# Optimization experiments

Hardware: AMD Instinct MI355X
Metric: run time of the kernel (lower is better)

Reference implementation:

```python
import jax, jax.numpy as jnp
import numpy as np

B, S, D_MODEL, D_K, D_V = 8, 2048, 1024, 512, 512


def setup_inputs() -> dict:
    key = jax.random.key(0)
    ks = jax.random.split(key, 7)
    sq = jax.random.normal(ks[0], (B, S, D_MODEL), dtype=jnp.float32)
    skv = jax.random.normal(ks[1], (B, S, D_MODEL), dtype=jnp.float32)
    q_pad = jax.random.uniform(ks[2], (B, S)) < 0.1
    kv_pad = jax.random.uniform(ks[3], (B, S)) < 0.1
    Wq = jax.random.normal(ks[4], (D_MODEL, D_K), dtype=jnp.float32) * (D_MODEL ** -0.5)
    Wk = jax.random.normal(ks[5], (D_MODEL, D_K), dtype=jnp.float32) * (D_MODEL ** -0.5)
    Wv = jax.random.normal(ks[6], (D_MODEL, D_V), dtype=jnp.float32) * (D_MODEL ** -0.5)
    return {
        "source_query": sq,
        "source_key_value": skv,
        "source_query_padding_mask": q_pad,
        "source_key_value_padding_mask": kv_pad,
        "Wq": Wq,
        "Wk": Wk,
        "Wv": Wv,
    }


def reference(source_query, source_key_value, source_query_padding_mask,
              source_key_value_padding_mask, Wq, Wk, Wv):
    neg_inf = jnp.float32(-jnp.inf)
    q = source_query @ Wq          # [B,Sq,d_k]
    k = source_key_value @ Wk      # [B,Sk,d_k]
    v = source_key_value @ Wv      # [B,Sk,d_v]
    scale = jnp.float32(D_K) ** -0.5
    scores = jnp.einsum("bqd,bkd->bqk", q, k) * scale  # [B,Sq,Sk]
    # query padding mask broadcast along key dim, kv padding mask along query dim
    pad = source_query_padding_mask[:, :, None] | source_key_value_padding_mask[:, None, :]
    scores = jnp.where(pad, neg_inf, scores)
    # causal mask (masked=True): positions above diagonal blocked
    Sq = scores.shape[1]
    causal = jnp.tril(jnp.ones((Sq, Sq), dtype=bool))
    scores = jnp.where(causal[None, :, :], scores, neg_inf)
    attn = jax.nn.softmax(scores, axis=-1)
    # fully-masked rows produce NaN -> zero (matches torch nan masked_fill)
    attn = jnp.where(jnp.isnan(attn), jnp.float32(0.0), attn)
    # dropout p=0.0 (eval): identity
    out = jnp.einsum("bqk,bkv->bqv", attn, v)  # [B,Sq,d_v]
    return out
```

## Files before the change

kernel.cpp:

```cpp
#include <hip/hip_runtime.h>

typedef unsigned short u16;
typedef unsigned int   u32;
typedef __attribute__((ext_vector_type(4))) float  f32x4;
typedef __attribute__((ext_vector_type(8))) __bf16 bf16x8;

#define BATCH 8
#define SEQ   2048
#define DMODEL 1024
#define DK    512
#define DV    512
#define SCALE 0.044194173824159216f

__device__ __forceinline__ u16 f2bf(float f) {
  u32 u = __float_as_uint(f);
  return (u16)((u + 0x7fffu + ((u >> 16) & 1u)) >> 16);
}

__device__ __forceinline__ bool read_mask(const void* p, int idx, int mode) {
  if (mode == 1) return ((const unsigned char*)p)[idx] != 0;
  if (mode == 2) return ((const float*)p)[idx] != 0.0f;
  return ((const int*)p)[idx] != 0;
}

__device__ __forceinline__ void gl_lds16(const u16* g, u16* l) {
  __builtin_amdgcn_global_load_lds(
      (const __attribute__((address_space(1))) u32*)g,
      (__attribute__((address_space(3))) u32*)l, 16, 0, 0);
}

__global__ void detect_mode(const int* __restrict__ qp, int* __restrict__ flag) {
  __shared__ int f;
  if (threadIdx.x == 0) f = 0;
  __syncthreads();
  int local = 0;
  for (int i = threadIdx.x; i < 4096; i += 256) {
    int v = qp[i];
    if (v == 0x3F800000) local |= 2;
    else if (v != 0 && v != 1 && v != -1) local |= 1;
  }
  if (local) atomicOr(&f, local);
  __syncthreads();
  if (threadIdx.x == 0) {
    int m = 0;
    if (f & 2) m = 2; else if (f & 1) m = 1;
    *flag = m;
  }
}

__global__ __launch_bounds__(256) void wt_transpose(const float* __restrict__ W0,
                                                    const float* __restrict__ W1,
                                                    const float* __restrict__ W2,
                                                    u16* __restrict__ dst) {
  const float* W = (blockIdx.z == 0) ? W0 : (blockIdx.z == 1) ? W1 : W2;
  u16* out = dst + (size_t)blockIdx.z * (DK * DMODEL);
  __shared__ float T[32][33];
  int k0 = blockIdx.x * 32, n0 = blockIdx.y * 32;
  int tx = threadIdx.x, ty = threadIdx.y;
#pragma unroll
  for (int i = 0; i < 4; ++i) {
    int r = ty + i * 8;
    T[r][tx] = W[(size_t)(k0 + r) * DK + n0 + tx];
  }
  __syncthreads();
#pragma unroll
  for (int i = 0; i < 4; ++i) {
    int r = ty + i * 8;
    out[(size_t)(n0 + r) * DMODEL + k0 + tx] = f2bf(T[tx][r]);
  }
}

__global__ __launch_bounds__(256) void convert_bf16(const float* __restrict__ src,
                                                    u16* __restrict__ dst) {
  int i = (blockIdx.x * 256 + threadIdx.x) * 8;
  f32x4 a = *(const f32x4*)(src + i);
  f32x4 b = *(const f32x4*)(src + i + 4);
  uint4 o;
  o.x = (u32)f2bf(a[0]) | ((u32)f2bf(a[1]) << 16);
  o.y = (u32)f2bf(a[2]) | ((u32)f2bf(a[3]) << 16);
  o.z = (u32)f2bf(b[0]) | ((u32)f2bf(b[1]) << 16);
  o.w = (u32)f2bf(b[2]) | ((u32)f2bf(b[3]) << 16);
  *(uint4*)(dst + i) = o;
}

__global__ __launch_bounds__(256, 3) void proj_gemm(const u16* __restrict__ A,
                                                    const u16* __restrict__ Wt_base,
                                                    int z0, u16* __restrict__ dst0,
                                                    u16* __restrict__ dst1) {
  int z = z0 + blockIdx.z;
  const u16* Wt = Wt_base + (size_t)z * (DK * DMODEL);
  u16* dst = (z == 2) ? dst1 : dst0;
  int n0 = blockIdx.x * 128, m0 = blockIdx.y * 128;

  __shared__ __align__(16) u16 As[128 * 64];
  __shared__ __align__(16) u16 Bs[128 * 64];

  int tid = threadIdx.x, lane = tid & 63, w = tid >> 6;
  int wm = w & 1, wn = w >> 1;
  int l15 = lane & 15, lg = lane >> 4;
  int r3 = lane >> 3, c7 = lane & 7;
  int csw = c7 ^ r3;

  f32x4 acc[4][4];
#pragma unroll
  for (int m = 0; m < 4; ++m)
#pragma unroll
    for (int n = 0; n < 4; ++n) acc[m][n] = (f32x4)0.0f;

  for (int k0 = 0; k0 < DMODEL; k0 += 64) {
    __syncthreads();
#pragma unroll
    for (int u = 0; u < 4; ++u) {
      int t = w * 4 + u;
      gl_lds16(A  + (size_t)(m0 + t * 8 + r3) * DMODEL + k0 + csw * 8, &As[t * 512]);
      gl_lds16(Wt + (size_t)(n0 + t * 8 + r3) * DMODEL + k0 + csw * 8, &Bs[t * 512]);
    }
    __syncthreads();
#pragma unroll
    for (int ks = 0; ks < 2; ++ks) {
      bf16x8 af[4], bfv[4];
#pragma unroll
      for (int m = 0; m < 4; ++m) {
        int row = wm * 64 + m * 16 + l15;
        af[m] = *(const bf16x8*)&As[row * 64 + (((ks * 4 + lg) ^ (l15 & 7)) * 8)];
      }
#pragma unroll
      for (int n = 0; n < 4; ++n) {
        int row = wn * 64 + n * 16 + l15;
        bfv[n] = *(const bf16x8*)&Bs[row * 64 + (((ks * 4 + lg) ^ (l15 & 7)) * 8)];
      }
#pragma unroll
      for (int m = 0; m < 4; ++m)
#pragma unroll
        for (int n = 0; n < 4; ++n)
          acc[m][n] = __builtin_amdgcn_mfma_f32_16x16x32_bf16(af[m], bfv[n], acc[m][n], 0, 0, 0);
    }
  }

  if (z != 2) {
#pragma unroll
    for (int m = 0; m < 4; ++m) {
      int rowb = m0 + wm * 64 + m * 16;
#pragma unroll
      for (int n = 0; n < 4; ++n) {
        int col = n0 + wn * 64 + n * 16 + l15;
        size_t base = (size_t)(rowb >> 4) * 8192 + (size_t)(col >> 5) * 512 + (col & 31);
#pragma unroll
        for (int r = 0; r < 4; ++r)
          dst[base + (lg * 4 + r) * 32] = f2bf(acc[m][n][r]);
      }
    }
  } else {
#pragma unroll
    for (int m = 0; m < 4; ++m) {
      int row0 = m0 + wm * 64 + m * 16 + lg * 4;
      int b = row0 >> 11, s0 = row0 & 2047;
#pragma unroll
      for (int n = 0; n < 4; ++n) {
        int dv = n0 + wn * 64 + n * 16 + l15;
        size_t off = (size_t)b * (SEQ * DV) + (size_t)(dv >> 4) * 32768 +
                     (size_t)(s0 >> 5) * 512 + (dv & 15) * 32 + (s0 & 31);
        u16 tmp[4] __attribute__((aligned(8)));
#pragma unroll
        for (int r = 0; r < 4; ++r) tmp[r] = f2bf(acc[m][n][r]);
        *(uint2*)&dst[off] = *(const uint2*)tmp;
      }
    }
  }
}

__global__ __launch_bounds__(256, 2) void attn_kernel(
    const u16* __restrict__ Qf, const u16* __restrict__ Kf,
    const u16* __restrict__ Vf, const void* __restrict__ qpad,
    const void* __restrict__ kvpad, const int* __restrict__ flag,
    float* __restrict__ out) {
  __shared__ __align__(16) u16 Pbuf[32 * 72];
  __shared__ float partm[32 * 2];
  __shared__ float ald[32];
  __shared__ float partl[32 * 2];

  int tid = threadIdx.x;
  int lane = tid & 63, w = tid >> 6;
  int l15 = lane & 15, lg = lane >> 4;
  int wk = w & 1;
  int m  = w >> 1;
  int bi = blockIdx.x;
  int j = bi & 63, b = bi >> 6;
  int qt = (j & 1) ? (63 - (j >> 1)) : (j >> 1);
  int q0 = qt * 32;
  int mode = *flag;
  int lanoff = l15 * 32 + lg * 8;

  const u16* Qb = Qf + (size_t)b * (SEQ * DK);
  const u16* Kb = Kf + (size_t)b * (SEQ * DK);
  const u16* Vb = Vf + (size_t)b * (SEQ * DV);

  bf16x8 qf[16];
  {
    const u16* qp = Qb + (size_t)(qt * 2 + m) * 8192 + lanoff;
#pragma unroll
    for (int ks = 0; ks < 16; ++ks) qf[ks] = *(const bf16x8*)(qp + ks * 512);
  }

  f32x4 o[2][8];
#pragma unroll
  for (int m2 = 0; m2 < 2; ++m2)
#pragma unroll
    for (int n = 0; n < 8; ++n) o[m2][n] = (f32x4)0.0f;

  float mo[4], lsum[4];
#pragma unroll
  for (int r = 0; r < 4; ++r) { mo[r] = -1e38f; lsum[r] = 0.0f; }

  int nkt = (q0 + 95) >> 6;

  for (int kt = 0; kt < nkt; ++kt) {
    int k0 = kt * 64;

    f32x4 s0 = (f32x4)0.0f, s1 = (f32x4)0.0f;
    {
      const u16* kp0 = Kb + (size_t)((k0 >> 4) + wk * 2) * 8192 + lanoff;
      const u16* kp1 = kp0 + 8192;
#pragma unroll
      for (int ks = 0; ks < 16; ++ks) {
        bf16x8 b0 = *(const bf16x8*)(kp0 + ks * 512);
        bf16x8 b1 = *(const bf16x8*)(kp1 + ks * 512);
        s0 = __builtin_amdgcn_mfma_f32_16x16x32_bf16(qf[ks], b0, s0, 0, 0, 0);
        s1 = __builtin_amdgcn_mfma_f32_16x16x32_bf16(qf[ks], b1, s1, 0, 0, 0);
      }
    }

    float sv[2][4];
#pragma unroll
    for (int kg = 0; kg < 2; ++kg) {
      int key = k0 + wk * 32 + kg * 16 + l15;
      bool kvm = read_mask(kvpad, b * SEQ + key, mode);
#pragma unroll
      for (int r = 0; r < 4; ++r) {
        int qrow = q0 + m * 16 + lg * 4 + r;
        float x = (kg == 0 ? s0[r] : s1[r]) * SCALE;
        sv[kg][r] = (kvm || key > qrow) ? -__builtin_inff() : x;
      }
    }

    float wmax[4];
#pragma unroll
    for (int r = 0; r < 4; ++r) wmax[r] = fmaxf(sv[0][r], sv[1][r]);
#pragma unroll
    for (int d = 1; d < 16; d <<= 1)
#pragma unroll
      for (int r = 0; r < 4; ++r) wmax[r] = fmaxf(wmax[r], __shfl_xor(wmax[r], d));
    if (l15 == 0) {
#pragma unroll
      for (int r = 0; r < 4; ++r) partm[(m * 16 + lg * 4 + r) * 2 + wk] = wmax[r];
    }
    __syncthreads();

    float al[4], ws[4];
#pragma unroll
    for (int r = 0; r < 4; ++r) {
      int row = m * 16 + lg * 4 + r;
      float tm = fmaxf(partm[row * 2], partm[row * 2 + 1]);
      float mn = fmaxf(mo[r], fmaxf(tm, -1e38f));
      al[r] = __expf(mo[r] - mn);
      mo[r] = mn;
      float p0 = __expf(sv[0][r] - mn);
      float p1 = __expf(sv[1][r] - mn);
      Pbuf[row * 72 + wk * 32 + l15] = f2bf(p0);
      Pbuf[row * 72 + wk * 32 + 16 + l15] = f2bf(p1);
      ws[r] = p0 + p1;
    }
#pragma unroll
    for (int d = 1; d < 16; d <<= 1)
#pragma unroll
      for (int r = 0; r < 4; ++r) ws[r] += __shfl_xor(ws[r], d);
#pragma unroll
    for (int r = 0; r < 4; ++r) lsum[r] = lsum[r] * al[r] + ws[r];
    if (wk == 0 && l15 == 0) {
#pragma unroll
      for (int r = 0; r < 4; ++r) ald[m * 16 + lg * 4 + r] = al[r];
    }
    __syncthreads();

    float ar[2][4];
#pragma unroll
    for (int m2 = 0; m2 < 2; ++m2)
#pragma unroll
      for (int r = 0; r < 4; ++r) ar[m2][r] = ald[m2 * 16 + lg * 4 + r];
#pragma unroll
    for (int m2 = 0; m2 < 2; ++m2)
#pragma unroll
      for (int n = 0; n < 8; ++n)
#pragma unroll
        for (int r = 0; r < 4; ++r) o[m2][n][r] *= ar[m2][r];

    {
      const u16* vpb = Vb + (size_t)(w * 8) * 32768 + (size_t)(k0 >> 5) * 512 + lanoff;
#pragma unroll
      for (int ks = 0; ks < 2; ++ks) {
        bf16x8 pa0 = *(const bf16x8*)&Pbuf[(l15) * 72 + ks * 32 + lg * 8];
        bf16x8 pa1 = *(const bf16x8*)&Pbuf[(16 + l15) * 72 + ks * 32 + lg * 8];
#pragma unroll
        for (int n = 0; n < 4; ++n) {
          bf16x8 bv0 = *(const bf16x8*)(vpb + (size_t)(n * 2) * 32768 + ks * 512);
          bf16x8 bv1 = *(const bf16x8*)(vpb + (size_t)(n * 2 + 1) * 32768 + ks * 512);
          o[0][n * 2]     = __builtin_amdgcn_mfma_f32_16x16x32_bf16(pa0, bv0, o[0][n * 2], 0, 0, 0);
          o[1][n * 2]     = __builtin_amdgcn_mfma_f32_16x16x32_bf16(pa1, bv0, o[1][n * 2], 0, 0, 0);
          o[0][n * 2 + 1] = __builtin_amdgcn_mfma_f32_16x16x32_bf16(pa0, bv1, o[0][n * 2 + 1], 0, 0, 0);
          o[1][n * 2 + 1] = __builtin_amdgcn_mfma_f32_16x16x32_bf16(pa1, bv1, o[1][n * 2 + 1], 0, 0, 0);
        }
      }
    }
  }

  if (l15 == 0) {
#pragma unroll
    for (int r = 0; r < 4; ++r) partl[(m * 16 + lg * 4 + r) * 2 + wk] = lsum[r];
  }
  __syncthreads();
  {
    float f[2][4];
#pragma unroll
    for (int m2 = 0; m2 < 2; ++m2)
#pragma unroll
      for (int r = 0; r < 4; ++r) {
        int row = m2 * 16 + lg * 4 + r;
        float l = partl[row * 2] + partl[row * 2 + 1];
        bool qp = read_mask(qpad, b * SEQ + q0 + row, mode);
        f[m2][r] = (l > 0.0f && !qp) ? 1.0f / l : 0.0f;
      }
#pragma unroll
    for (int m2 = 0; m2 < 2; ++m2)
#pragma unroll
      for (int n = 0; n < 8; ++n) {
        int dv = w * 128 + n * 16 + l15;
#pragma unroll
        for (int r = 0; r < 4; ++r) {
          int row = m2 * 16 + lg * 4 + r;
          out[(size_t)(b * SEQ + q0 + row) * DV + dv] = o[m2][n][r] * f[m2][r];
        }
      }
  }
}

extern "C" void kernel_launch(void* const* d_in, const int* in_sizes, int n_in,
                              void* d_out, int out_size, void* d_ws, size_t ws_size,
                              hipStream_t stream) {
  const float* sq  = (const float*)d_in[0];
  const float* skv = (const float*)d_in[1];
  const void* qp   = d_in[2];
  const void* kvp  = d_in[3];
  const float* Wq  = (const float*)d_in[4];
  const float* Wk  = (const float*)d_in[5];
  const float* Wv  = (const float*)d_in[6];
  char* ws = (char*)d_ws;

  u16* Abf = (u16*)ws;
  u16* Qf  = (u16*)(ws + 33554432);
  u16* Kf  = (u16*)(ws + 50331648);
  u16* Vf  = (u16*)(ws + 67108864);
  u16* Wt  = (u16*)(ws + 83886080);
  int* flag = (int*)(ws + 87031808);

  wt_transpose<<<dim3(32, 16, 3), dim3(32, 8, 1), 0, stream>>>(Wq, Wk, Wv, Wt);
  detect_mode<<<1, 256, 0, stream>>>((const int*)qp, flag);

  convert_bf16<<<8192, 256, 0, stream>>>(sq, Abf);
  proj_gemm<<<dim3(4, 128, 1), dim3(256), 0, stream>>>(Abf, Wt, 0, Qf, Qf);

  convert_bf16<<<8192, 256, 0, stream>>>(skv, Abf);
  proj_gemm<<<dim3(4, 128, 2), dim3(256), 0, stream>>>(Abf, Wt, 1, Kf, Vf);

  attn_kernel<<<dim3(512), dim3(256), 0, stream>>>(Qf, Kf, Vf, qp, kvp, flag,
                                                   (float*)d_out);
}
```

Baseline: 479.5 us.

## Split attention block across eight waves with Q staged in LDS

The attention kernel moves from 4 to 8 waves per block. Each wave now computes a 16-key slice of the score tile and a 64-column slice of the output, and the Q tile is staged once into shared memory via direct global-to-LDS loads instead of being held in registers per wave. Every wave recomputes the row rescale factors from the per-row partial maxima, which removes the separate alpha broadcast buffer. The batch-major block order is also replaced with an interleaved batch/tile mapping for load balance. This is meant to raise parallelism and lower register pressure, at the cost of more LDS traffic for Q and more block-wide barrier participants.

```diff
diff --git a/kernel.cpp b/kernel.cpp
--- a/kernel.cpp
+++ b/kernel.cpp
@@ -169,24 +169,25 @@
   }
 }
 
-__global__ __launch_bounds__(256, 2) void attn_kernel(
+__global__ __launch_bounds__(512, 4) void attn_kernel(
     const u16* __restrict__ Qf, const u16* __restrict__ Kf,
     const u16* __restrict__ Vf, const void* __restrict__ qpad,
     const void* __restrict__ kvpad, const int* __restrict__ flag,
     float* __restrict__ out) {
+  __shared__ __align__(16) u16 Qs[32 * 512];
   __shared__ __align__(16) u16 Pbuf[32 * 72];
-  __shared__ float partm[32 * 2];
-  __shared__ float ald[32];
-  __shared__ float partl[32 * 2];
+  __shared__ float partm[32 * 4];
+  __shared__ float partl[32 * 4];
 
   int tid = threadIdx.x;
   int lane = tid & 63, w = tid >> 6;
   int l15 = lane & 15, lg = lane >> 4;
-  int wk = w & 1;
-  int m  = w >> 1;
+  int wk = w & 3;
+  int m  = w >> 2;
   int bi = blockIdx.x;
-  int j = bi & 63, b = bi >> 6;
-  int qt = (j & 1) ? (63 - (j >> 1)) : (j >> 1);
+  int b = bi & 7, j = bi >> 3;
+  int c = j & 31, h = j >> 5;
+  int qt = ((c ^ h) & 1) ? (63 - c) : c;
   int q0 = qt * 32;
   int mode = *flag;
   int lanoff = l15 * 32 + lg * 8;
@@ -195,119 +196,123 @@
   const u16* Kb = Kf + (size_t)b * (SEQ * DK);
   const u16* Vb = Vf + (size_t)b * (SEQ * DV);
 
-  bf16x8 qf[16];
   {
-    const u16* qp = Qb + (size_t)(qt * 2 + m) * 8192 + lanoff;
-#pragma unroll
-    for (int ks = 0; ks < 16; ++ks) qf[ks] = *(const bf16x8*)(qp + ks * 512);
-  }
-
-  f32x4 o[2][8];
-#pragma unroll
-  for (int m2 = 0; m2 < 2; ++m2)
-#pragma unroll
-    for (int n = 0; n < 8; ++n) o[m2][n] = (f32x4)0.0f;
-
-  float mo[4], lsum[4];
-#pragma unroll
-  for (int r = 0; r < 4; ++r) { mo[r] = -1e38f; lsum[r] = 0.0f; }
+    const u16* qsrc = Qb + (size_t)qt * 16384 + lane * 8;
+#pragma unroll
+    for (int u = 0; u < 4; ++u) {
+      int i = w * 4 + u;
+      gl_lds16(qsrc + i * 512, &Qs[i * 512]);
+    }
+  }
+
+  f32x4 o[2][4];
+#pragma unroll
+  for (int mf = 0; mf < 2; ++mf)
+#pragma unroll
+    for (int n = 0; n < 4; ++n) o[mf][n] = (f32x4)0.0f;
+
+  float mo[2][4], lsum[4];
+#pragma unroll
+  for (int mf = 0; mf < 2; ++mf)
+#pragma unroll
+    for (int r = 0; r < 4; ++r) mo[mf][r] = -1e38f;
+#pragma unroll
+  for (int r = 0; r < 4; ++r) lsum[r] = 0.0f;
 
   int nkt = (q0 + 95) >> 6;
+  __syncthreads();
 
   for (int kt = 0; kt < nkt; ++kt) {
     int k0 = kt * 64;
-
-    f32x4 s0 = (f32x4)0.0f, s1 = (f32x4)0.0f;
+    int key = k0 + wk * 16 + l15;
+    bool kvm = read_mask(kvpad, b * SEQ + key, mode);
+
+    f32x4 sa = (f32x4)0.0f, sb = (f32x4)0.0f;
     {
-      const u16* kp0 = Kb + (size_t)((k0 >> 4) + wk * 2) * 8192 + lanoff;
-      const u16* kp1 = kp0 + 8192;
-#pragma unroll
-      for (int ks = 0; ks < 16; ++ks) {
-        bf16x8 b0 = *(const bf16x8*)(kp0 + ks * 512);
-        bf16x8 b1 = *(const bf16x8*)(kp1 + ks * 512);
-        s0 = __builtin_amdgcn_mfma_f32_16x16x32_bf16(qf[ks], b0, s0, 0, 0, 0);
-        s1 = __builtin_amdgcn_mfma_f32_16x16x32_bf16(qf[ks], b1, s1, 0, 0, 0);
-      }
-    }
-
-    float sv[2][4];
-#pragma unroll
-    for (int kg = 0; kg < 2; ++kg) {
-      int key = k0 + wk * 32 + kg * 16 + l15;
-      bool kvm = read_mask(kvpad, b * SEQ + key, mode);
-#pragma unroll
-      for (int r = 0; r < 4; ++r) {
-        int qrow = q0 + m * 16 + lg * 4 + r;
-        float x = (kg == 0 ? s0[r] : s1[r]) * SCALE;
-        sv[kg][r] = (kvm || key > qrow) ? -__builtin_inff() : x;
-      }
+      const u16* kp = Kb + (size_t)((k0 >> 4) + wk) * 8192 + lanoff;
+      const u16* qp = &Qs[m * 8192 + lanoff];
+#pragma unroll
+      for (int ks = 0; ks < 16; ks += 2) {
+        bf16x8 qv0 = *(const bf16x8*)(qp + ks * 512);
+        bf16x8 kv0 = *(const bf16x8*)(kp + ks * 512);
+        bf16x8 qv1 = *(const bf16x8*)(qp + (ks + 1) * 512);
+        bf16x8 kv1 = *(const bf16x8*)(kp + (ks + 1) * 512);
+        sa = __builtin_amdgcn_mfma_f32_16x16x32_bf16(qv0, kv0, sa, 0, 0, 0);
+        sb = __builtin_amdgcn_mfma_f32_16x16x32_bf16(qv1, kv1, sb, 0, 0, 0);
+      }
+    }
+
+    float sv[4];
+#pragma unroll
+    for (int r = 0; r < 4; ++r) {
+      int qrow = q0 + m * 16 + lg * 4 + r;
+      float x = (sa[r] + sb[r]) * SCALE;
+      sv[r] = (kvm || key > qrow) ? -__builtin_inff() : x;
     }
 
     float wmax[4];
 #pragma unroll
-    for (int r = 0; r < 4; ++r) wmax[r] = fmaxf(sv[0][r], sv[1][r]);
+    for (int r = 0; r < 4; ++r) wmax[r] = sv[r];
 #pragma unroll
     for (int d = 1; d < 16; d <<= 1)
 #pragma unroll
       for (int r = 0; r < 4; ++r) wmax[r] = fmaxf(wmax[r], __shfl_xor(wmax[r], d));
     if (l15 == 0) {
 #pragma unroll
-      for (int r = 0; r < 4; ++r) partm[(m * 16 + lg * 4 + r) * 2 + wk] = wmax[r];
+      for (int r = 0; r < 4; ++r) partm[(m * 16 + lg * 4 + r) * 4 + wk] = wmax[r];
     }
     __syncthreads();
 
-    float al[4], ws[4];
+    float al[2][4];
+#pragma unroll
+    for (int mf = 0; mf < 2; ++mf)
+#pragma unroll
+      for (int r = 0; r < 4; ++r) {
+        int row = mf * 16 + lg * 4 + r;
+        float tm = fmaxf(fmaxf(partm[row * 4 + 0], partm[row * 4 + 1]),
+                         fmaxf(partm[row * 4 + 2], partm[row * 4 + 3]));
+        float mn = fmaxf(mo[mf][r], fmaxf(tm, -1e38f));
+        al[mf][r] = __expf(mo[mf][r] - mn);
+        mo[mf][r] = mn;
+      }
+    float ws[4];
 #pragma unroll
     for (int r = 0; r < 4; ++r) {
       int row = m * 16 + lg * 4 + r;
-      float tm = fmaxf(partm[row * 2], partm[row * 2 + 1]);
-      float mn = fmaxf(mo[r], fmaxf(tm, -1e38f));
-      al[r] = __expf(mo[r] - mn);
-      mo[r] = mn;
-      float p0 = __expf(sv[0][r] - mn);
-      float p1 = __expf(sv[1][r] - mn);
-      Pbuf[row * 72 + wk * 32 + l15] = f2bf(p0);
-      Pbuf[row * 72 + wk * 32 + 16 + l15] = f2bf(p1);
-      ws[r] = p0 + p1;
+      float p = __expf(sv[r] - mo[m][r]);
+      Pbuf[row * 72 + wk * 16 + l15] = f2bf(p);
+      ws[r] = p;
     }
 #pragma unroll
     for (int d = 1; d < 16; d <<= 1)
 #pragma unroll
       for (int r = 0; r < 4; ++r) ws[r] += __shfl_xor(ws[r], d);
 #pragma unroll
-    for (int r = 0; r < 4; ++r) lsum[r] = lsum[r] * al[r] + ws[r];
-    if (wk == 0 && l15 == 0) {
-#pragma unroll
-      for (int r = 0; r < 4; ++r) ald[m * 16 + lg * 4 + r] = al[r];
-    }
+    for (int r = 0; r < 4; ++r) lsum[r] = lsum[r] * al[m][r] + ws[r];
     __syncthreads();
 
-    float ar[2][4];
-#pragma unroll
-    for (int m2 = 0; m2 < 2; ++m2)
-#pragma unroll
-      for (int r = 0; r < 4; ++r) ar[m2][r] = ald[m2 * 16 + lg * 4 + r];
-#pragma unroll
-    for (int m2 = 0; m2 < 2; ++m2)
-#pragma unroll
-      for (int n = 0; n < 8; ++n)
-#pragma unroll
-        for (int r = 0; r < 4; ++r) o[m2][n][r] *= ar[m2][r];
+#pragma unroll
+    for (int mf = 0; mf < 2; ++mf)
+#pragma unroll
+      for (int n = 0; n < 4; ++n)
+#pragma unroll
+        for (int r = 0; r < 4; ++r) o[mf][n][r] *= al[mf][r];
 
     {
-      const u16* vpb = Vb + (size_t)(w * 8) * 32768 + (size_t)(k0 >> 5) * 512 + lanoff;
+      bf16x8 pa0[2], pa1[2];
 #pragma unroll
       for (int ks = 0; ks < 2; ++ks) {
-        bf16x8 pa0 = *(const bf16x8*)&Pbuf[(l15) * 72 + ks * 32 + lg * 8];
-        bf16x8 pa1 = *(const bf16x8*)&Pbuf[(16 + l15) * 72 + ks * 32 + lg * 8];
-#pragma unroll
-        for (int n = 0; n < 4; ++n) {
-          bf16x8 bv0 = *(const bf16x8*)(vpb + (size_t)(n * 2) * 32768 + ks * 512);
-          bf16x8 bv1 = *(const bf16x8*)(vpb + (size_t)(n * 2 + 1) * 32768 + ks * 512);
-          o[0][n * 2]     = __builtin_amdgcn_mfma_f32_16x16x32_bf16(pa0, bv0, o[0][n * 2], 0, 0, 0);
-          o[1][n * 2]     = __builtin_amdgcn_mfma_f32_16x16x32_bf16(pa1, bv0, o[1][n * 2], 0, 0, 0);
-          o[0][n * 2 + 1] = __builtin_amdgcn_mfma_f32_16x16x32_bf16(pa0, bv1, o[0][n * 2 + 1], 0, 0, 0);
-          o[1][n * 2 + 1] = __builtin_amdgcn_mfma_f32_16x16x32_bf16(pa1, bv1, o[1][n * 2 + 1], 0, 0, 0);
+        pa0[ks] = *(const bf16x8*)&Pbuf[l15 * 72 + ks * 32 + lg * 8];
+        pa1[ks] = *(const bf16x8*)&Pbuf[(16 + l15) * 72 + ks * 32 + lg * 8];
+      }
+      const u16* vp = Vb + (size_t)(w * 4) * 32768 + (size_t)(k0 >> 5) * 512 + lanoff;
+#pragma unroll
+      for (int n = 0; n < 4; ++n) {
+#pragma unroll
+        for (int ks = 0; ks < 2; ++ks) {
+          bf16x8 bv = *(const bf16x8*)(vp + (size_t)n * 32768 + ks * 512);
+          o[0][n] = __builtin_amdgcn_mfma_f32_16x16x32_bf16(pa0[ks], bv, o[0][n], 0, 0, 0);
+          o[1][n] = __builtin_amdgcn_mfma_f32_16x16x32_bf16(pa1[ks], bv, o[1][n], 0, 0, 0);
         }
       }
     }
@@ -315,29 +320,30 @@
 
   if (l15 == 0) {
 #pragma unroll
-    for (int r = 0; r < 4; ++r) partl[(m * 16 + lg * 4 + r) * 2 + wk] = lsum[r];
+    for (int r = 0; r < 4; ++r) partl[(m * 16 + lg * 4 + r) * 4 + wk] = lsum[r];
   }
   __syncthreads();
   {
     float f[2][4];
 #pragma unroll
-    for (int m2 = 0; m2 < 2; ++m2)
+    for (int mf = 0; mf < 2; ++mf)
 #pragma unroll
       for (int r = 0; r < 4; ++r) {
-        int row = m2 * 16 + lg * 4 + r;
-        float l = partl[row * 2] + partl[row * 2 + 1];
+        int row = mf * 16 + lg * 4 + r;
+        float l = partl[row * 4 + 0] + partl[row * 4 + 1] +
+                  partl[row * 4 + 2] + partl[row * 4 + 3];
         bool qp = read_mask(qpad, b * SEQ + q0 + row, mode);
-        f[m2][r] = (l > 0.0f && !qp) ? 1.0f / l : 0.0f;
-      }
-#pragma unroll
-    for (int m2 = 0; m2 < 2; ++m2)
-#pragma unroll
-      for (int n = 0; n < 8; ++n) {
-        int dv = w * 128 + n * 16 + l15;
+        f[mf][r] = (l > 0.0f && !qp) ? 1.0f / l : 0.0f;
+      }
+#pragma unroll
+    for (int mf = 0; mf < 2; ++mf)
+#pragma unroll
+      for (int n = 0; n < 4; ++n) {
+        int dv = w * 64 + n * 16 + l15;
 #pragma unroll
         for (int r = 0; r < 4; ++r) {
-          int row = m2 * 16 + lg * 4 + r;
-          out[(size_t)(b * SEQ + q0 + row) * DV + dv] = o[m2][n][r] * f[m2][r];
+          int row = mf * 16 + lg * 4 + r;
+          out[(size_t)(b * SEQ + q0 + row) * DV + dv] = o[mf][n][r] * f[mf][r];
         }
       }
   }
@@ -371,6 +377,6 @@
   convert_bf16<<<8192, 256, 0, stream>>>(skv, Abf);
   proj_gemm<<<dim3(4, 128, 2), dim3(256), 0, stream>>>(Abf, Wt, 1, Kf, Vf);
 
-  attn_kernel<<<dim3(512), dim3(256), 0, stream>>>(Qf, Kf, Vf, qp, kvp, flag,
+  attn_kernel<<<dim3(512), dim3(512), 0, stream>>>(Qf, Kf, Vf, qp, kvp, flag,
                                                    (float*)d_out);
 }
```

New measurement: 447.6 us. 1.07x faster.
